# Kernel tuning notes

Measured on AMD Instinct MI355X. Metric: run time of the kernel, lower is better.

## Reference

```python
import jax, jax.numpy as jnp
import numpy as np

NX, NY, NT = 128, 128, 16
NC = 8
NRAD = 2 * NY * 8  # 2*Ny*n_spokes, n_spokes = 8


def setup_inputs() -> dict:
    key = jax.random.key(0)
    k1, k2, k3, k4 = jax.random.split(key, 4)
    x = jax.random.normal(k1, (2, NX, NY, NT), dtype=jnp.float32)
    # radial k-space trajectory coordinates in radians [-pi, pi]
    ktraj = (jax.random.uniform(k2, (2, NRAD, NT), dtype=jnp.float32) * 2.0 - 1.0) * np.float32(np.pi)
    csmap = jax.random.normal(k3, (NC, 2, NX, NY), dtype=jnp.float32)
    dcomp = jax.random.uniform(k4, (NRAD, NT), dtype=jnp.float32)  # density compensation weights > 0
    return {"x": x, "ktraj": ktraj, "csmap": csmap, "dcomp": dcomp}


def _adaga(x, ktraj, csmap, dcomp):
    """Frame-wise E^H D E (apply_AdagA): sense NUFFT fwd, dcomp weighting, adjoint.

    Exact NDFT is used as the reference for the Kaiser-Bessel gridded NUFFT.
    The phase factor is separable per k-point: exp(-i(kx*x + ky*y)) = Ex[k,x]*Ey[k,y],
    so we never materialize the full (Nrad, Nx*Ny) DFT matrix.
    """
    Nx, Ny, Nt = x.shape[1], x.shape[2], x.shape[3]
    img = x[0] + 1j * x[1]                      # (Nx,Ny,Nt) complex64
    smap = csmap[:, 0] + 1j * csmap[:, 1]       # (Nc,Nx,Ny)
    xs = (jnp.arange(Nx) - Nx // 2).astype(jnp.float32)  # centered pixel grid
    ys = (jnp.arange(Ny) - Ny // 2).astype(jnp.float32)
    scale = np.float32(1.0 / np.sqrt(Nx * Ny))  # 'ortho' normalization

    def frame(img_t, k_t, d_t):
        kx, ky = k_t[0], k_t[1]                              # (Nrad,)
        Ex = jnp.exp(-1j * kx[:, None] * xs[None, :])        # (Nrad,Nx)
        Ey = jnp.exp(-1j * ky[:, None] * ys[None, :])        # (Nrad,Ny)
        src = smap * img_t[None]                             # (Nc,Nx,Ny)
        # forward NDFT (type-2): kdat[c,k] = sum_{x,y} src[c,x,y] Ex[k,x] Ey[k,y]
        t = jnp.einsum('kx,cxy->cky', Ex, src)               # (Nc,Nrad,Ny)
        kdat = jnp.einsum('ky,cky->ck', Ey, t) * scale       # (Nc,Nrad)
        # density compensation
        g = kdat * d_t[None, :]                              # (Nc,Nrad)
        # adjoint NDFT (type-1) + coil combine with conj sensitivities
        t2 = jnp.einsum('ky,ck->cky', jnp.conj(Ey), g)       # (Nc,Nrad,Ny)
        xim = jnp.einsum('kx,cky->cxy', jnp.conj(Ex), t2) * scale  # (Nc,Nx,Ny)
        return jnp.sum(jnp.conj(smap) * xim, axis=0)         # (Nx,Ny)

    out = jax.vmap(frame, in_axes=(2, 2, 1), out_axes=2)(img, ktraj, dcomp)  # (Nx,Ny,Nt)
    return jnp.stack([out.real, out.imag], axis=0)           # (2,Nx,Ny,Nt)


def reference(x, ktraj, csmap, dcomp):
    return _adaga(x, ktraj, csmap, dcomp)
```

## Files before the change

kernel.cpp:

```cpp
#include <hip/hip_runtime.h>


#define NT 16
#define NK 2048
#define NXY 128
#define NC 8

typedef _Float16 f16x8 __attribute__((ext_vector_type(8)));
typedef float f32x4 __attribute__((ext_vector_type(4)));

union F8 { f16x8 h; uint u[4]; };

#define MFMA16(a, b, c) __builtin_amdgcn_mfma_f32_16x16x32_f16((a), (b), (c), 0, 0, 0)

__device__ __forceinline__ uint pack2h(float a, float b) {
    union { _Float16 h[2]; uint u; } p;
    p.h[0] = (_Float16)a; p.h[1] = (_Float16)b;
    return p.u;
}
__device__ __forceinline__ float2 unpack2h(uint v) {
    union { uint u; _Float16 h[2]; } p;
    p.u = v;
    return make_float2((float)p.h[0], (float)p.h[1]);
}
__device__ __forceinline__ uint rot16(uint v) { return (v >> 16) | (v << 16); }

__global__ __launch_bounds__(256) void prep_phasA(const float* __restrict__ ktraj,
                                                  uint* __restrict__ ExC,
                                                  uint* __restrict__ EyL) {
    const int t = blockIdx.x;
    const int k = blockIdx.y * 2 + (threadIdx.x >> 7);
    const int x = threadIdx.x & 127;
    const float kx = ktraj[(size_t)k * NT + t];
    const float ky = ktraj[(size_t)(NK + k) * NT + t];
    const float xm = (float)(x - 64);
    float s, c;
    __sincosf(-kx * xm, &s, &c);
    ExC[((size_t)(t * 16 + (k >> 7)) * 8 + (x >> 4)) * 2048 +
        (size_t)(k & 127) * 16 + (x & 15)] = pack2h(c, s);
    __sincosf(-ky * xm, &s, &c);
    EyL[((size_t)t * NK + k) * NXY + x] = pack2h(c, s);
}

__global__ __launch_bounds__(256) void prep_phasB(const float* __restrict__ ktraj,
                                                  uint* __restrict__ ExT) {
    const int t = blockIdx.x, x = blockIdx.y;
    const int k = blockIdx.z * 256 + threadIdx.x;
    const float kx = ktraj[(size_t)k * NT + t];
    float s, c;
    __sincosf(-kx * (float)(x - 64), &s, &c);
    ExT[((size_t)t * NXY + x) * NK + k] = pack2h(c, s);
}

__global__ __launch_bounds__(256) void prep_src(const float* __restrict__ xin,
                                                const float* __restrict__ csmap,
                                                uint* __restrict__ srcB) {
    const int idx = blockIdx.x * 256 + threadIdx.x;
    const int t = idx & 15, r = (idx >> 4) & 15, xl = (idx >> 8) & 15,
              mf = (idx >> 12) & 7, ch = (idx >> 15) & 7, c = idx >> 18;
    const int x = ch * 16 + xl, y = mf * 16 + r;
    const float ir = xin[(size_t)(x * NXY + y) * NT + t];
    const float ii = xin[(size_t)NXY * NXY * NT + (size_t)(x * NXY + y) * NT + t];
    const float sr = csmap[(size_t)c * 2 * NXY * NXY + x * NXY + y];
    const float si = csmap[(size_t)c * 2 * NXY * NXY + NXY * NXY + x * NXY + y];
    srcB[((size_t)(t * NC + c) << 14) + ch * 2048 + mf * 256 + r * 16 + xl] =
        pack2h(sr * ir - si * ii, sr * ii + si * ir);
}

__global__ __launch_bounds__(256, 2) void fwd_gemm(const uint* __restrict__ ExC,
                                                   const uint* __restrict__ EyL,
                                                   const uint* __restrict__ srcB,
                                                   const float* __restrict__ dcomp,
                                                   float2* __restrict__ g) {
    const int t = blockIdx.x, c = blockIdx.y, kt = blockIdx.z;
    const int tid = threadIdx.x, lane = tid & 63, ws = tid >> 6;
    const int quad = lane >> 4, l15 = lane & 15;
    const int mh = ws >> 1, nq = ws & 1;

    __shared__ __align__(16) _Float16 As[2][4096];

    f32x4 accr[4][2], acci[4][2];
#pragma unroll
    for (int mf = 0; mf < 4; ++mf)
#pragma unroll
        for (int nf = 0; nf < 2; ++nf) { accr[mf][nf] = (f32x4)0.0f; acci[mf][nf] = (f32x4)0.0f; }

    const uint* srcT = srcB + ((size_t)(t * NC + c) << 14);
    const uint* exB = ExC + (size_t)(t * 16 + (kt >> 1)) * 16384;
    const int kin0 = (kt & 1) * 64 + nq * 32;

    F8 vA0 = *(const F8*)(srcT + tid * 8);
    F8 vA1 = *(const F8*)(srcT + tid * 8 + 4);
    F8 Bc0 = *(const F8*)(exB + (kin0 + l15) * 16 + quad * 4);
    F8 Bc1 = *(const F8*)(exB + (kin0 + 16 + l15) * 16 + quad * 4);

#pragma unroll 2
    for (int ch = 0; ch < 8; ++ch) {
        const int buf = ch & 1;
        *(F8*)&As[buf][tid * 16] = vA0;
        *(F8*)&As[buf][tid * 16 + 8] = vA1;
        __syncthreads();
        const int chn = ch < 7 ? ch + 1 : 7;
        vA0 = *(const F8*)(srcT + chn * 2048 + tid * 8);
        vA1 = *(const F8*)(srcT + chn * 2048 + tid * 8 + 4);
        F8 Bn0 = *(const F8*)(exB + chn * 2048 + (kin0 + l15) * 16 + quad * 4);
        F8 Bn1 = *(const F8*)(exB + chn * 2048 + (kin0 + 16 + l15) * 16 + quad * 4);
        __builtin_amdgcn_sched_barrier(0);
        F8 Br0, Bi0, Br1, Bi1;
#pragma unroll
        for (int d = 0; d < 4; ++d) {
            Br0.u[d] = Bc0.u[d] ^ 0x80000000u;
            Bi0.u[d] = rot16(Bc0.u[d]);
            Br1.u[d] = Bc1.u[d] ^ 0x80000000u;
            Bi1.u[d] = rot16(Bc1.u[d]);
        }
#pragma unroll
        for (int mf = 0; mf < 4; ++mf) {
            F8 Ap = *(const F8*)&As[buf][(mh * 4 + mf) * 512 + l15 * 32 + quad * 8];
            accr[mf][0] = MFMA16(Ap.h, Br0.h, accr[mf][0]);
            acci[mf][0] = MFMA16(Ap.h, Bi0.h, acci[mf][0]);
            accr[mf][1] = MFMA16(Ap.h, Br1.h, accr[mf][1]);
            acci[mf][1] = MFMA16(Ap.h, Bi1.h, acci[mf][1]);
        }
        Bc0 = Bn0; Bc1 = Bn1;
    }

    __syncthreads();
    float* red = (float*)(&As[0][0]);
#pragma unroll
    for (int nf = 0; nf < 2; ++nf) {
        const int kin = kin0 + nf * 16 + l15;
        const int kpoint = (kt >> 1) * 128 + kin;
        const uint* eyRow = EyL + ((size_t)t * NK + kpoint) * NXY;
        float kdr = 0.f, kdi = 0.f;
#pragma unroll
        for (int mf = 0; mf < 4; ++mf) {
            const int yc = mh * 4 + mf;
            F8 e4 = *(const F8*)(eyRow + yc * 16 + quad * 4);
#pragma unroll
            for (int rr = 0; rr < 4; ++rr) {
                float2 ey = unpack2h(e4.u[rr]);
                float cr = accr[mf][nf][rr], ci = acci[mf][nf][rr];
                kdr += ey.x * cr - ey.y * ci;
                kdi += ey.x * ci + ey.y * cr;
            }
        }
        kdr += __shfl_xor(kdr, 16); kdr += __shfl_xor(kdr, 32);
        kdi += __shfl_xor(kdi, 16); kdi += __shfl_xor(kdi, 32);
        if (lane < 16) {
            const int kl = nq * 32 + nf * 16 + l15;
            red[(mh * 64 + kl) * 2] = kdr;
            red[(mh * 64 + kl) * 2 + 1] = kdi;
        }
    }
    __syncthreads();
    if (tid < 64) {
        const int kpoint = kt * 64 + tid;
        const float kdr = red[tid * 2] + red[(64 + tid) * 2];
        const float kdi = red[tid * 2 + 1] + red[(64 + tid) * 2 + 1];
        const float w = dcomp[(size_t)kpoint * NT + t] * (1.0f / 16384.0f);
        g[((size_t)t * NK + kpoint) * NC + c] = make_float2(kdr * w, kdi * w);
    }
}

__global__ __launch_bounds__(512) void adj_gemm(const uint* __restrict__ ExT,
                                                const uint* __restrict__ EyL,
                                                const float2* __restrict__ g,
                                                const float* __restrict__ csmap,
                                                float* __restrict__ out) {
    const int t = blockIdx.x, yt = blockIdx.y, ybase = yt * 8;
    const int tid = threadIdx.x, lane = tid & 63, ws = tid >> 6;
    const int quad = lane >> 4, l15 = lane & 15;
    const int x = ws * 16 + l15;

    __shared__ __align__(16) _Float16 Ts[2][64][72];

    f32x4 accr[4], acci[4];
#pragma unroll
    for (int mf = 0; mf < 4; ++mf) { accr[mf] = (f32x4)0.0f; acci[mf] = (f32x4)0.0f; }

    const float2* gBase = g + (size_t)t * NK * NC;
    const uint* eyBase = EyL + (size_t)t * NK * NXY;
    const uint* exRow = ExT + (size_t)t * NXY * NK + (size_t)x * NK;

    const int bm = tid & 63;
    const int bk4 = (tid >> 6) * 4;
    const int by = ybase + (bm >> 3), bc = bm & 7;

    {
        F8 w;
#pragma unroll
        for (int j = 0; j < 4; ++j) {
            int kp = bk4 + j;
            float2 gv = gBase[kp * NC + bc];
            float2 ey = unpack2h(eyBase[(size_t)kp * NXY + by]);
            w.u[j] = pack2h(ey.x * gv.x + ey.y * gv.y, ey.x * gv.y - ey.y * gv.x);
        }
        *(F8*)&Ts[0][bm][bk4 * 2] = w;
    }
    __syncthreads();

    for (int ch = 0; ch < 64; ++ch) {
        const int buf = ch & 1;
        const int chn = ch < 63 ? ch + 1 : 63;
        const int kb = chn * 32 + bk4;
        float2 gv0 = gBase[(kb + 0) * NC + bc];
        float2 gv1 = gBase[(kb + 1) * NC + bc];
        float2 gv2 = gBase[(kb + 2) * NC + bc];
        float2 gv3 = gBase[(kb + 3) * NC + bc];
        uint ev0 = eyBase[(size_t)(kb + 0) * NXY + by];
        uint ev1 = eyBase[(size_t)(kb + 1) * NXY + by];
        uint ev2 = eyBase[(size_t)(kb + 2) * NXY + by];
        uint ev3 = eyBase[(size_t)(kb + 3) * NXY + by];
        F8 Bf0 = *(const F8*)(exRow + ch * 32 + quad * 4);
        F8 Bf1 = *(const F8*)(exRow + ch * 32 + 16 + quad * 4);
        F8 Bi0, Bi1;
#pragma unroll
        for (int d = 0; d < 4; ++d) {
            Bi0.u[d] = rot16(Bf0.u[d]) ^ 0x00008000u;
            Bi1.u[d] = rot16(Bf1.u[d]) ^ 0x00008000u;
        }
#pragma unroll
        for (int mf = 0; mf < 4; ++mf) {
            F8 Ap0 = *(const F8*)&Ts[buf][mf * 16 + l15][quad * 8];
            accr[mf] = MFMA16(Ap0.h, Bf0.h, accr[mf]);
            acci[mf] = MFMA16(Ap0.h, Bi0.h, acci[mf]);
            F8 Ap1 = *(const F8*)&Ts[buf][mf * 16 + l15][32 + quad * 8];
            accr[mf] = MFMA16(Ap1.h, Bf1.h, accr[mf]);
            acci[mf] = MFMA16(Ap1.h, Bi1.h, acci[mf]);
        }
        {
            F8 w; float2 e;
            e = unpack2h(ev0); w.u[0] = pack2h(e.x*gv0.x + e.y*gv0.y, e.x*gv0.y - e.y*gv0.x);
            e = unpack2h(ev1); w.u[1] = pack2h(e.x*gv1.x + e.y*gv1.y, e.x*gv1.y - e.y*gv1.x);
            e = unpack2h(ev2); w.u[2] = pack2h(e.x*gv2.x + e.y*gv2.y, e.x*gv2.y - e.y*gv2.x);
            e = unpack2h(ev3); w.u[3] = pack2h(e.x*gv3.x + e.y*gv3.y, e.x*gv3.y - e.y*gv3.x);
            *(F8*)&Ts[buf ^ 1][bm][bk4 * 2] = w;
        }
        __syncthreads();
    }

#pragma unroll
    for (int mf = 0; mf < 4; ++mf) {
        const int y = ybase + 2 * mf + (quad >> 1);
        float or_ = 0.f, oi_ = 0.f;
#pragma unroll
        for (int r = 0; r < 4; ++r) {
            int c = 4 * (quad & 1) + r;
            float sr = csmap[(size_t)c * 2 * NXY * NXY + x * NXY + y];
            float si = csmap[(size_t)c * 2 * NXY * NXY + NXY * NXY + x * NXY + y];
            float xr = accr[mf][r], xi = acci[mf][r];
            or_ += sr * xr + si * xi;
            oi_ += sr * xi - si * xr;
        }
        or_ += __shfl_xor(or_, 16);
        oi_ += __shfl_xor(oi_, 16);
        if ((lane & 16) == 0) {
            out[(size_t)(x * NXY + y) * NT + t] = or_;
            out[(size_t)NXY * NXY * NT + (size_t)(x * NXY + y) * NT + t] = oi_;
        }
    }
}

extern "C" void kernel_launch(void* const* d_in, const int* in_sizes, int n_in,
                              void* d_out, int out_size, void* d_ws, size_t ws_size,
                              hipStream_t stream) {
    const float* xin   = (const float*)d_in[0];
    const float* ktraj = (const float*)d_in[1];
    const float* csmap = (const float*)d_in[2];
    const float* dcomp = (const float*)d_in[3];
    float* out = (float*)d_out;

    const size_t TBL = (size_t)NT * NK * NXY;
    uint* ExC  = (uint*)d_ws;
    uint* ExT  = ExC + TBL;
    uint* EyL  = ExT + TBL;
    uint* srcB = EyL + TBL;
    float2* g  = (float2*)(srcB + (size_t)NT * NC * NXY * NXY);

    prep_phasA<<<dim3(NT, NK / 2), 256, 0, stream>>>(ktraj, ExC, EyL);
    prep_phasB<<<dim3(NT, NXY, NK / 256), 256, 0, stream>>>(ktraj, ExT);
    prep_src<<<dim3(8192), 256, 0, stream>>>(xin, csmap, srcB);
    fwd_gemm<<<dim3(NT, NC, 32), 256, 0, stream>>>(ExC, EyL, srcB, dcomp, g);
    adj_gemm<<<dim3(NT, NXY / 8), 512, 0, stream>>>(ExT, EyL, g, csmap, out);
}
```

Baseline: 234.0 us.

## Merge prep kernels into one launch and re-tile fwd_gemm warps over k

Measured after the change: 221.3 us. 5.5% less time.

```diff
diff --git a/kernel.cpp b/kernel.cpp
--- a/kernel.cpp
+++ b/kernel.cpp
@@ -25,46 +25,48 @@
 }
 __device__ __forceinline__ uint rot16(uint v) { return (v >> 16) | (v << 16); }
 
-__global__ __launch_bounds__(256) void prep_phasA(const float* __restrict__ ktraj,
-                                                  uint* __restrict__ ExC,
-                                                  uint* __restrict__ EyL) {
-    const int t = blockIdx.x;
-    const int k = blockIdx.y * 2 + (threadIdx.x >> 7);
-    const int x = threadIdx.x & 127;
-    const float kx = ktraj[(size_t)k * NT + t];
-    const float ky = ktraj[(size_t)(NK + k) * NT + t];
-    const float xm = (float)(x - 64);
-    float s, c;
-    __sincosf(-kx * xm, &s, &c);
-    ExC[((size_t)(t * 16 + (k >> 7)) * 8 + (x >> 4)) * 2048 +
-        (size_t)(k & 127) * 16 + (x & 15)] = pack2h(c, s);
-    __sincosf(-ky * xm, &s, &c);
-    EyL[((size_t)t * NK + k) * NXY + x] = pack2h(c, s);
-}
-
-__global__ __launch_bounds__(256) void prep_phasB(const float* __restrict__ ktraj,
-                                                  uint* __restrict__ ExT) {
-    const int t = blockIdx.x, x = blockIdx.y;
-    const int k = blockIdx.z * 256 + threadIdx.x;
-    const float kx = ktraj[(size_t)k * NT + t];
-    float s, c;
-    __sincosf(-kx * (float)(x - 64), &s, &c);
-    ExT[((size_t)t * NXY + x) * NK + k] = pack2h(c, s);
-}
-
-__global__ __launch_bounds__(256) void prep_src(const float* __restrict__ xin,
+__global__ __launch_bounds__(256) void prep_all(const float* __restrict__ ktraj,
+                                                const float* __restrict__ xin,
                                                 const float* __restrict__ csmap,
+                                                uint* __restrict__ ExC,
+                                                uint* __restrict__ ExT,
+                                                uint* __restrict__ EyL,
                                                 uint* __restrict__ srcB) {
-    const int idx = blockIdx.x * 256 + threadIdx.x;
-    const int t = idx & 15, r = (idx >> 4) & 15, xl = (idx >> 8) & 15,
-              mf = (idx >> 12) & 7, ch = (idx >> 15) & 7, c = idx >> 18;
-    const int x = ch * 16 + xl, y = mf * 16 + r;
-    const float ir = xin[(size_t)(x * NXY + y) * NT + t];
-    const float ii = xin[(size_t)NXY * NXY * NT + (size_t)(x * NXY + y) * NT + t];
-    const float sr = csmap[(size_t)c * 2 * NXY * NXY + x * NXY + y];
-    const float si = csmap[(size_t)c * 2 * NXY * NXY + NXY * NXY + x * NXY + y];
-    srcB[((size_t)(t * NC + c) << 14) + ch * 2048 + mf * 256 + r * 16 + xl] =
-        pack2h(sr * ir - si * ii, sr * ii + si * ir);
+    const int b = blockIdx.x;
+    const int tid = threadIdx.x;
+    if (b < 16384) {
+        const int t = b >> 10;
+        const int k = (b & 1023) * 2 + (tid >> 7);
+        const int x = tid & 127;
+        const float kx = ktraj[(size_t)k * NT + t];
+        const float ky = ktraj[(size_t)(NK + k) * NT + t];
+        const float xm = (float)(x - 64);
+        float s, c;
+        __sincosf(-kx * xm, &s, &c);
+        ExC[((size_t)(t * 16 + (k >> 7)) * 8 + (x >> 4)) * 2048 +
+            (size_t)(k & 127) * 16 + (x & 15)] = pack2h(c, s);
+        __sincosf(-ky * xm, &s, &c);
+        EyL[((size_t)t * NK + k) * NXY + x] = pack2h(c, s);
+    } else if (b < 32768) {
+        const int q = b - 16384;
+        const int t = q >> 10, x = (q >> 3) & 127, kz = q & 7;
+        const int k = kz * 256 + tid;
+        const float kx = ktraj[(size_t)k * NT + t];
+        float s, c;
+        __sincosf(-kx * (float)(x - 64), &s, &c);
+        ExT[((size_t)t * NXY + x) * NK + k] = pack2h(c, s);
+    } else {
+        const int idx = (b - 32768) * 256 + tid;
+        const int t = idx & 15, r = (idx >> 4) & 15, xl = (idx >> 8) & 15,
+                  mf = (idx >> 12) & 7, ch = (idx >> 15) & 7, c = idx >> 18;
+        const int x = ch * 16 + xl, y = mf * 16 + r;
+        const float ir = xin[(size_t)(x * NXY + y) * NT + t];
+        const float ii = xin[(size_t)NXY * NXY * NT + (size_t)(x * NXY + y) * NT + t];
+        const float sr = csmap[(size_t)c * 2 * NXY * NXY + x * NXY + y];
+        const float si = csmap[(size_t)c * 2 * NXY * NXY + NXY * NXY + x * NXY + y];
+        srcB[((size_t)(t * NC + c) << 14) + ch * 2048 + mf * 256 + r * 16 + xl] =
+            pack2h(sr * ir - si * ii, sr * ii + si * ir);
+    }
 }
 
 __global__ __launch_bounds__(256, 2) void fwd_gemm(const uint* __restrict__ ExC,
@@ -75,24 +77,20 @@
     const int t = blockIdx.x, c = blockIdx.y, kt = blockIdx.z;
     const int tid = threadIdx.x, lane = tid & 63, ws = tid >> 6;
     const int quad = lane >> 4, l15 = lane & 15;
-    const int mh = ws >> 1, nq = ws & 1;
 
     __shared__ __align__(16) _Float16 As[2][4096];
 
-    f32x4 accr[4][2], acci[4][2];
-#pragma unroll
-    for (int mf = 0; mf < 4; ++mf)
-#pragma unroll
-        for (int nf = 0; nf < 2; ++nf) { accr[mf][nf] = (f32x4)0.0f; acci[mf][nf] = (f32x4)0.0f; }
+    f32x4 accr[8], acci[8];
+#pragma unroll
+    for (int mf = 0; mf < 8; ++mf) { accr[mf] = (f32x4)0.0f; acci[mf] = (f32x4)0.0f; }
 
     const uint* srcT = srcB + ((size_t)(t * NC + c) << 14);
     const uint* exB = ExC + (size_t)(t * 16 + (kt >> 1)) * 16384;
-    const int kin0 = (kt & 1) * 64 + nq * 32;
+    const int kin0 = (kt & 1) * 64 + ws * 16;
 
     F8 vA0 = *(const F8*)(srcT + tid * 8);
     F8 vA1 = *(const F8*)(srcT + tid * 8 + 4);
-    F8 Bc0 = *(const F8*)(exB + (kin0 + l15) * 16 + quad * 4);
-    F8 Bc1 = *(const F8*)(exB + (kin0 + 16 + l15) * 16 + quad * 4);
+    F8 Bc = *(const F8*)(exB + (kin0 + l15) * 16 + quad * 4);
 
 #pragma unroll 2
     for (int ch = 0; ch < 8; ++ch) {
@@ -103,62 +101,41 @@
         const int chn = ch < 7 ? ch + 1 : 7;
         vA0 = *(const F8*)(srcT + chn * 2048 + tid * 8);
         vA1 = *(const F8*)(srcT + chn * 2048 + tid * 8 + 4);
-        F8 Bn0 = *(const F8*)(exB + chn * 2048 + (kin0 + l15) * 16 + quad * 4);
-        F8 Bn1 = *(const F8*)(exB + chn * 2048 + (kin0 + 16 + l15) * 16 + quad * 4);
+        F8 Bn = *(const F8*)(exB + chn * 2048 + (kin0 + l15) * 16 + quad * 4);
         __builtin_amdgcn_sched_barrier(0);
-        F8 Br0, Bi0, Br1, Bi1;
+        F8 Br, Bi;
 #pragma unroll
         for (int d = 0; d < 4; ++d) {
-            Br0.u[d] = Bc0.u[d] ^ 0x80000000u;
-            Bi0.u[d] = rot16(Bc0.u[d]);
-            Br1.u[d] = Bc1.u[d] ^ 0x80000000u;
-            Bi1.u[d] = rot16(Bc1.u[d]);
-        }
-#pragma unroll
-        for (int mf = 0; mf < 4; ++mf) {
-            F8 Ap = *(const F8*)&As[buf][(mh * 4 + mf) * 512 + l15 * 32 + quad * 8];
-            accr[mf][0] = MFMA16(Ap.h, Br0.h, accr[mf][0]);
-            acci[mf][0] = MFMA16(Ap.h, Bi0.h, acci[mf][0]);
-            accr[mf][1] = MFMA16(Ap.h, Br1.h, accr[mf][1]);
-            acci[mf][1] = MFMA16(Ap.h, Bi1.h, acci[mf][1]);
-        }
-        Bc0 = Bn0; Bc1 = Bn1;
-    }
-
-    __syncthreads();
-    float* red = (float*)(&As[0][0]);
-#pragma unroll
-    for (int nf = 0; nf < 2; ++nf) {
-        const int kin = kin0 + nf * 16 + l15;
-        const int kpoint = (kt >> 1) * 128 + kin;
-        const uint* eyRow = EyL + ((size_t)t * NK + kpoint) * NXY;
-        float kdr = 0.f, kdi = 0.f;
-#pragma unroll
-        for (int mf = 0; mf < 4; ++mf) {
-            const int yc = mh * 4 + mf;
-            F8 e4 = *(const F8*)(eyRow + yc * 16 + quad * 4);
-#pragma unroll
-            for (int rr = 0; rr < 4; ++rr) {
-                float2 ey = unpack2h(e4.u[rr]);
-                float cr = accr[mf][nf][rr], ci = acci[mf][nf][rr];
-                kdr += ey.x * cr - ey.y * ci;
-                kdi += ey.x * ci + ey.y * cr;
-            }
-        }
-        kdr += __shfl_xor(kdr, 16); kdr += __shfl_xor(kdr, 32);
-        kdi += __shfl_xor(kdi, 16); kdi += __shfl_xor(kdi, 32);
-        if (lane < 16) {
-            const int kl = nq * 32 + nf * 16 + l15;
-            red[(mh * 64 + kl) * 2] = kdr;
-            red[(mh * 64 + kl) * 2 + 1] = kdi;
-        }
-    }
-    __syncthreads();
-    if (tid < 64) {
-        const int kpoint = kt * 64 + tid;
-        const float kdr = red[tid * 2] + red[(64 + tid) * 2];
-        const float kdi = red[tid * 2 + 1] + red[(64 + tid) * 2 + 1];
-        const float w = dcomp[(size_t)kpoint * NT + t] * (1.0f / 16384.0f);
+            Br.u[d] = Bc.u[d] ^ 0x80000000u;
+            Bi.u[d] = rot16(Bc.u[d]);
+        }
+#pragma unroll
+        for (int mf = 0; mf < 8; ++mf) {
+            F8 Ap = *(const F8*)&As[buf][mf * 512 + l15 * 32 + quad * 8];
+            accr[mf] = MFMA16(Ap.h, Br.h, accr[mf]);
+            acci[mf] = MFMA16(Ap.h, Bi.h, acci[mf]);
+        }
+        Bc = Bn;
+    }
+
+    const int kpoint = kt * 64 + ws * 16 + l15;
+    const uint* eyRow = EyL + ((size_t)t * NK + kpoint) * NXY;
+    float kdr = 0.f, kdi = 0.f;
+#pragma unroll
+    for (int mf = 0; mf < 8; ++mf) {
+        F8 e4 = *(const F8*)(eyRow + mf * 16 + quad * 4);
+#pragma unroll
+        for (int rr = 0; rr < 4; ++rr) {
+            float2 ey = unpack2h(e4.u[rr]);
+            float cr = accr[mf][rr], ci = acci[mf][rr];
+            kdr += ey.x * cr - ey.y * ci;
+            kdi += ey.x * ci + ey.y * cr;
+        }
+    }
+    kdr += __shfl_xor(kdr, 16); kdr += __shfl_xor(kdr, 32);
+    kdi += __shfl_xor(kdi, 16); kdi += __shfl_xor(kdi, 32);
+    if (lane < 16) {
+        float w = dcomp[(size_t)kpoint * NT + t] * (1.0f / 16384.0f);
         g[((size_t)t * NK + kpoint) * NC + c] = make_float2(kdr * w, kdi * w);
     }
 }
@@ -278,9 +255,7 @@
     uint* srcB = EyL + TBL;
     float2* g  = (float2*)(srcB + (size_t)NT * NC * NXY * NXY);
 
-    prep_phasA<<<dim3(NT, NK / 2), 256, 0, stream>>>(ktraj, ExC, EyL);
-    prep_phasB<<<dim3(NT, NXY, NK / 256), 256, 0, stream>>>(ktraj, ExT);
-    prep_src<<<dim3(8192), 256, 0, stream>>>(xin, csmap, srcB);
+    prep_all<<<dim3(40960), 256, 0, stream>>>(ktraj, xin, csmap, ExC, ExT, EyL, srcB);
     fwd_gemm<<<dim3(NT, NC, 32), 256, 0, stream>>>(ExC, EyL, srcB, dcomp, g);
     adj_gemm<<<dim3(NT, NXY / 8), 512, 0, stream>>>(ExT, EyL, g, csmap, out);
 }
```
